# Kernel optimization log

Hardware: AMD Instinct MI355X
Metric: run time of the kernel (lower is better)

The kernel has to match this reference:

```python
import jax, jax.numpy as jnp
import numpy as np

B, DIM, NH, HD, H, W = 4, 64, 8, 8, 256, 256  # head_dim must equal num_heads (scale broadcast)


def setup_inputs() -> dict:
    key = jax.random.key(0)
    ks = jax.random.split(key, 10)
    s = 0.05
    return {
        "x": jax.random.normal(ks[0], (B, DIM, H, W), jnp.float32),
        "w3": jax.random.normal(ks[1], (DIM, 1, 3, 3), jnp.float32) * s,  # depthwise 3x3
        "b3": jax.random.normal(ks[2], (DIM,), jnp.float32) * s,
        "w5": jax.random.normal(ks[3], (DIM, 1, 5, 5), jnp.float32) * s,  # depthwise 5x5
        "b5": jax.random.normal(ks[4], (DIM,), jnp.float32) * s,
        "wqkv": jax.random.normal(ks[5], (3 * DIM, DIM), jnp.float32) * s,  # 1x1 conv, no bias
        "scale": jnp.ones((NH, 1, 1), jnp.float32),
        "g1_w": jax.random.normal(ks[6], (DIM // 4, DIM), jnp.float32) * s,
        "g1_b": jnp.zeros((DIM // 4,), jnp.float32),
        "g2_w": jax.random.normal(ks[7], (2, DIM // 4), jnp.float32) * s,
        "g2_b": jnp.zeros((2,), jnp.float32),
        "wp": jax.random.normal(ks[8], (DIM, DIM), jnp.float32) * s,  # 1x1 proj
        "bp": jnp.zeros((DIM,), jnp.float32),
    }


def _dwconv(x, w, b, pad):
    out = jax.lax.conv_general_dilated(
        x, w, (1, 1), [(pad, pad), (pad, pad)],
        dimension_numbers=("NCHW", "OIHW", "NCHW"), feature_group_count=x.shape[1])
    return out + b[None, :, None, None]


def _l2norm(t, eps=1e-12):  # F.normalize(dim=-1)
    n = jnp.sqrt(jnp.sum(t * t, axis=-1, keepdims=True))
    return t / jnp.maximum(n, eps)


def reference(x, w3, b3, w5, b5, wqkv, scale, g1_w, g1_b, g2_w, g2_b, wp, bp):
    b, c, h, w = x.shape
    conv_feat = _dwconv(x, w3, b3, 1) + _dwconv(x, w5, b5, 2)

    qkv = jnp.einsum("oc,bchw->bohw", wqkv, x)          # [b,3c,h,w]
    qkv = qkv.reshape(b, 3, NH, HD, h * w)
    q, k, v = qkv[:, 0], qkv[:, 1], qkv[:, 2]           # [b,NH,HD,hw]
    q = _l2norm(q)
    k = _l2norm(k)

    q_h = q.reshape(b, NH, HD, h, w)
    k_h = k.reshape(b, NH, HD, h, w)
    v_h = v.reshape(b, NH, HD, h, w)

    # row-axis attention: per (b,head,d-channel) attention over rows x (scale broadcasts onto HD axis)
    attn_h = jnp.einsum("bhdxy,bhdzy->bhdxz", q_h, k_h) * scale   # [b,NH,HD,h,h]
    attn_h = jax.nn.softmax(attn_h, axis=-1)
    out_h = jnp.einsum("bhdxz,bhdzy->bhdxy", attn_h, v_h).reshape(b, c, h, w)

    # column-axis attention (operate on transposed spatial layout)
    q_v = jnp.swapaxes(q_h, -1, -2)                      # [b,NH,HD,w,h]
    k_v = jnp.swapaxes(k_h, -1, -2)
    v_v = jnp.swapaxes(v_h, -1, -2)
    attn_v = jnp.einsum("bhdyx,bhdzx->bhdyz", q_v, k_v) * scale   # [b,NH,HD,w,w]
    attn_v = jax.nn.softmax(attn_v, axis=-1)
    out_v = jnp.einsum("bhdyz,bhdzx->bhdyx", attn_v, v_v)         # [b,NH,HD,w,h]
    out_v = jnp.swapaxes(out_v, -1, -2).reshape(b, c, h, w)

    attn_feat = out_h + out_v

    # global-pool gating: softmax over 2 mixing weights
    gx = jnp.mean(x, axis=(2, 3))                        # [b,c]
    h1 = jax.nn.relu(gx @ g1_w.T + g1_b)
    gw = jax.nn.softmax(h1 @ g2_w.T + g2_b, axis=1)      # [b,2]
    cw = gw[:, 0][:, None, None, None]
    aw = gw[:, 1][:, None, None, None]

    out = cw * conv_feat + aw * attn_feat
    return jnp.einsum("oc,bchw->bohw", wp, out) + bp[None, :, None, None]
```

## Files before the change

### kernel.cpp

```cpp
#include <hip/hip_runtime.h>
#include <stdint.h>


typedef unsigned short u16;
typedef __attribute__((ext_vector_type(8))) short bf16x8;
typedef __attribute__((ext_vector_type(4))) float f32x4;

#define DEV static __device__ __forceinline__

DEV u16 f2bf(float f) {
  unsigned u = __float_as_uint(f);
  return (u16)((u + 0x7fffu + ((u >> 16) & 1u)) >> 16);
}
DEV float bf2f(u16 h) { return __uint_as_float(((unsigned)h) << 16); }

DEV void bar_lds() {
  asm volatile("s_waitcnt lgkmcnt(0)" ::: "memory");
  __builtin_amdgcn_s_barrier();
}

__global__ void k_gx(const float* __restrict__ x, float* __restrict__ gxsum) {
  int bc = blockIdx.x, t = threadIdx.x;
  const float4* p = (const float4*)(x + ((size_t)bc << 16));
  float s = 0.f;
  for (int i = 0; i < 64; ++i) { float4 v = p[t + 256 * i]; s += v.x + v.y + v.z + v.w; }
  for (int off = 32; off; off >>= 1) s += __shfl_down(s, off);
  __shared__ float lds[4];
  if ((t & 63) == 0) lds[t >> 6] = s;
  __syncthreads();
  if (t == 0) gxsum[bc] = lds[0] + lds[1] + lds[2] + lds[3];
}

__global__ void k_gate(const float* __restrict__ gxsum, const float* __restrict__ g1w,
                       const float* __restrict__ g1b, const float* __restrict__ g2w,
                       const float* __restrict__ g2b, float* __restrict__ cwaw) {
  __shared__ float h1[4][16];
  int t = threadIdx.x;
  int b = t >> 4, j = t & 15;
  float a = g1b[j];
  for (int c = 0; c < 64; ++c) a += g1w[j * 64 + c] * gxsum[b * 64 + c] * (1.f / 65536.f);
  h1[b][j] = fmaxf(a, 0.f);
  __syncthreads();
  if (t < 4) {
    float l0 = g2b[0], l1 = g2b[1];
    for (int k = 0; k < 16; ++k) { l0 += g2w[k] * h1[t][k]; l1 += g2w[16 + k] * h1[t][k]; }
    float m = fmaxf(l0, l1);
    float e0 = __expf(l0 - m), e1 = __expf(l1 - m);
    float inv = 1.f / (e0 + e1);
    cwaw[t * 2 + 0] = e0 * inv;
    cwaw[t * 2 + 1] = e1 * inv;
  }
}

__global__ __launch_bounds__(256) void k_qkv(const float* __restrict__ x,
                                             const float* __restrict__ wqkv,
                                             u16* __restrict__ qkv) {
  __shared__ u16 Ws[192 * 72];
  __shared__ u16 Xs[128 * 72];
  int t = threadIdx.x;
  int b = blockIdx.x >> 9;
  int p0 = (blockIdx.x & 511) << 7;

  {
    int row = t >> 2, c0 = (t & 3) << 4;
#pragma unroll
    for (int i = 0; i < 3; ++i) {
      int r = i * 64 + row;
      const float* src = wqkv + r * 64 + c0;
      unsigned pk[8];
#pragma unroll
      for (int j = 0; j < 8; ++j)
        pk[j] = (unsigned)f2bf(src[2 * j]) | ((unsigned)f2bf(src[2 * j + 1]) << 16);
      uint4* dst = (uint4*)&Ws[r * 72 + c0];
      dst[0] = make_uint4(pk[0], pk[1], pk[2], pk[3]);
      dst[1] = make_uint4(pk[4], pk[5], pk[6], pk[7]);
    }
  }
  {
    int p = t & 127, ch = t >> 7;
    const float* xb = x + ((size_t)(b * 64) << 16) + p0 + p;
#pragma unroll
    for (int i = 0; i < 32; ++i) {
      int c = 2 * i + ch;
      Xs[p * 72 + c] = f2bf(xb[(size_t)c << 16]);
    }
  }
  __syncthreads();

  int w = t >> 6, l = t & 63, q = l >> 4, cl = l & 15;
  bf16x8 af[3][2];
#pragma unroll
  for (int g = 0; g < 3; ++g)
#pragma unroll
    for (int k = 0; k < 2; ++k)
      af[g][k] = *(const bf16x8*)&Ws[(w * 48 + g * 16 + cl) * 72 + k * 32 + q * 8];

  f32x4 acc[3][8];
  f32x4 zero = {0.f, 0.f, 0.f, 0.f};
#pragma unroll
  for (int g = 0; g < 3; ++g)
#pragma unroll
    for (int j = 0; j < 8; ++j) acc[g][j] = zero;

  for (int j = 0; j < 8; ++j) {
    bf16x8 b0 = *(const bf16x8*)&Xs[(j * 16 + cl) * 72 + q * 8];
    bf16x8 b1 = *(const bf16x8*)&Xs[(j * 16 + cl) * 72 + 32 + q * 8];
#pragma unroll
    for (int g = 0; g < 3; ++g) {
      acc[g][j] = __builtin_amdgcn_mfma_f32_16x16x32_bf16(af[g][0], b0, acc[g][j], 0, 0, 0);
      acc[g][j] = __builtin_amdgcn_mfma_f32_16x16x32_bf16(af[g][1], b1, acc[g][j], 0, 0, 0);
    }
  }
  u16* outb = qkv + ((size_t)(b * 192) << 16) + p0;
  for (int g = 0; g < 3; ++g) {
    int rowb = w * 48 + g * 16 + q * 4;
#pragma unroll
    for (int r = 0; r < 4; ++r) {
      u16* orow = outb + ((size_t)(rowb + r) << 16);
#pragma unroll
      for (int j = 0; j < 8; ++j) orow[j * 16 + cl] = f2bf(acc[g][j][r]);
    }
  }
}

__global__ void k_rnorm(const u16* __restrict__ qkv, float* __restrict__ rnorm) {
  int b = blockIdx.x >> 7, ch = blockIdx.x & 127;
  const uint2* p2 = (const uint2*)(qkv + ((size_t)(b * 192 + ch) << 16));
  int t = threadIdx.x;
  float s = 0.f;
  for (int i = 0; i < 64; ++i) {
    uint2 v = p2[t + 256 * i];
    float a = bf2f(v.x & 0xffff), bq = bf2f(v.x >> 16);
    float c = bf2f(v.y & 0xffff), d = bf2f(v.y >> 16);
    s += a * a + bq * bq + c * c + d * d;
  }
  for (int off = 32; off; off >>= 1) s += __shfl_down(s, off);
  __shared__ float lds[4];
  if ((t & 63) == 0) lds[t >> 6] = s;
  __syncthreads();
  if (t == 0) {
    float tot = lds[0] + lds[1] + lds[2] + lds[3];
    rnorm[blockIdx.x] = 1.f / fmaxf(sqrtf(tot), 1e-12f);
  }
}

__global__ void k_conv(const float* __restrict__ x, const float* __restrict__ w3,
                       const float* __restrict__ b3, const float* __restrict__ w5,
                       const float* __restrict__ b5, const float* __restrict__ cwaw,
                       float* __restrict__ outmix) {
  int rt = blockIdx.x & 31, bc = blockIdx.x >> 5, c = bc & 63, b = bc >> 6;
  int r0 = rt * 8;
  const float* xp = x + ((size_t)bc << 16);
  __shared__ float xs[12][260];
  int y = threadIdx.x;
  for (int rr = 0; rr < 12; ++rr) {
    int gr = r0 - 2 + rr;
    xs[rr][y + 2] = (gr >= 0 && gr < 256) ? xp[(size_t)gr * 256 + y] : 0.f;
  }
  if (y < 2) {
    for (int rr = 0; rr < 12; ++rr) { xs[rr][y] = 0.f; xs[rr][258 + y] = 0.f; }
  }
  __syncthreads();
  float W3[9], W5[25];
#pragma unroll
  for (int i = 0; i < 9; ++i) W3[i] = w3[c * 9 + i];
#pragma unroll
  for (int i = 0; i < 25; ++i) W5[i] = w5[c * 25 + i];
  float bias = b3[c] + b5[c];
  float cw = cwaw[b * 2];
  float* op = outmix + ((size_t)bc << 16);
  for (int k = 0; k < 8; ++k) {
    float a = bias;
#pragma unroll
    for (int di = 0; di < 3; ++di)
#pragma unroll
      for (int dj = 0; dj < 3; ++dj)
        a += W3[di * 3 + dj] * xs[k + 1 + di][y + 1 + dj];
#pragma unroll
    for (int di = 0; di < 5; ++di)
#pragma unroll
      for (int dj = 0; dj < 5; ++dj)
        a += W5[di * 5 + dj] * xs[k + di][y + dj];
    op[(size_t)(r0 + k) * 256 + y] = cw * a;
  }
}

__global__ __launch_bounds__(256) void k_attn(
    const u16* __restrict__ qkv, const float* __restrict__ rnorm,
    const float* __restrict__ scale, u16* __restrict__ oh, u16* __restrict__ ov) {
  __shared__ __align__(16) unsigned char smem[54272];
  u16* Pls = (u16*)smem;
  unsigned* Qt32 = (unsigned*)smem;
  float* red = (float*)(smem + 33792);
  unsigned* Tt32 = (unsigned*)(smem + 33792);
  float* Osf = (float*)smem;

  int t = threadIdx.x;
  int w = t >> 6, l = t & 63, q = l >> 4, cl = l & 15;
  int idx = (blockIdx.x & 7) * 256 + (blockIdx.x >> 3);
  int rt = idx & 3, dir = (idx >> 2) & 1, c = (idx >> 3) & 63, b = idx >> 9;
  int r0 = rt << 6;

  const size_t P = 65536;
  const u16* Qp = qkv + (size_t)(b * 192 + c) * P;
  const u16* Kp = qkv + (size_t)(b * 192 + 64 + c) * P;
  const u16* Vp = qkv + (size_t)(b * 192 + 128 + c) * P;

  float sc = rnorm[b * 128 + c] * rnorm[b * 128 + 64 + c] * scale[c >> 3];

  f32x4 Sa[4][4];
  f32x4 zero = {0.f, 0.f, 0.f, 0.f};
#pragma unroll
  for (int i = 0; i < 4; ++i)
#pragma unroll
    for (int j = 0; j < 4; ++j) Sa[i][j] = zero;

  if (dir == 0) {
    for (int yw = 0; yw < 8; ++yw) {
      int y0 = yw << 5;
      bf16x8 af[4], bfr[4];
#pragma unroll
      for (int i = 0; i < 4; ++i)
        af[i] = *(const bf16x8*)&Qp[(size_t)(r0 + i * 16 + cl) * 256 + y0 + q * 8];
#pragma unroll
      for (int j = 0; j < 4; ++j)
        bfr[j] = *(const bf16x8*)&Kp[(size_t)(w * 64 + j * 16 + cl) * 256 + y0 + q * 8];
      __builtin_amdgcn_s_setprio(1);
#pragma unroll
      for (int i = 0; i < 4; ++i)
#pragma unroll
        for (int j = 0; j < 4; ++j)
          Sa[i][j] = __builtin_amdgcn_mfma_f32_16x16x32_bf16(af[i], bfr[j], Sa[i][j], 0, 0, 0);
      __builtin_amdgcn_s_setprio(0);
    }
  } else {
    int y2 = t >> 4, colc = t & 15;
    int kkey = (((y2 >> 2) ^ (colc & 3)) << 2) + (y2 & 3);
    int qkey = (((y2 >> 2) ^ ((colc >> 2) & 3)) << 2) + (y2 & 3);
    unsigned KA[8], KB[8], QA[2], QB[2];
    {
      const u16* krp = Kp + (size_t)(2 * y2) * 256 + colc * 16;
      uint4 ka0 = *(const uint4*)krp;
      uint4 ka1 = *(const uint4*)(krp + 8);
      uint4 kb0 = *(const uint4*)(krp + 256);
      uint4 kb1 = *(const uint4*)(krp + 264);
      const u16* qrp = Qp + (size_t)(2 * y2) * 256 + r0 + colc * 4;
      uint2 qa = *(const uint2*)qrp;
      uint2 qb = *(const uint2*)(qrp + 256);
      KA[0] = ka0.x; KA[1] = ka0.y; KA[2] = ka0.z; KA[3] = ka0.w;
      KA[4] = ka1.x; KA[5] = ka1.y; KA[6] = ka1.z; KA[7] = ka1.w;
      KB[0] = kb0.x; KB[1] = kb0.y; KB[2] = kb0.z; KB[3] = kb0.w;
      KB[4] = kb1.x; KB[5] = kb1.y; KB[6] = kb1.z; KB[7] = kb1.w;
      QA[0] = qa.x; QA[1] = qa.y; QB[0] = qb.x; QB[1] = qb.y;
    }
#pragma unroll
    for (int yw = 0; yw < 8; ++yw) {
      bar_lds();
#pragma unroll
      for (int m = 0; m < 16; ++m) {
        unsigned lo = (m & 1) ? (KA[m >> 1] >> 16) : (KA[m >> 1] & 0xffffu);
        unsigned hi = (m & 1) ? (KB[m >> 1] & 0xffff0000u) : (KB[m >> 1] << 16);
        Tt32[(colc * 16 + m) * 20 + kkey] = lo | hi;
      }
#pragma unroll
      for (int m = 0; m < 4; ++m) {
        unsigned lo = (m & 1) ? (QA[m >> 1] >> 16) : (QA[m >> 1] & 0xffffu);
        unsigned hi = (m & 1) ? (QB[m >> 1] & 0xffff0000u) : (QB[m >> 1] << 16);
        Qt32[(colc * 4 + m) * 20 + qkey] = lo | hi;
      }
      unsigned NKA[8], NKB[8], NQA[2], NQB[2];
      if (yw < 7) {
        int y0 = (yw + 1) << 5;
        const u16* krp = Kp + (size_t)(y0 + 2 * y2) * 256 + colc * 16;
        uint4 ka0 = *(const uint4*)krp;
        uint4 ka1 = *(const uint4*)(krp + 8);
        uint4 kb0 = *(const uint4*)(krp + 256);
        uint4 kb1 = *(const uint4*)(krp + 264);
        const u16* qrp = Qp + (size_t)(y0 + 2 * y2) * 256 + r0 + colc * 4;
        uint2 qa = *(const uint2*)qrp;
        uint2 qb = *(const uint2*)(qrp + 256);
        NKA[0] = ka0.x; NKA[1] = ka0.y; NKA[2] = ka0.z; NKA[3] = ka0.w;
        NKA[4] = ka1.x; NKA[5] = ka1.y; NKA[6] = ka1.z; NKA[7] = ka1.w;
        NKB[0] = kb0.x; NKB[1] = kb0.y; NKB[2] = kb0.z; NKB[3] = kb0.w;
        NKB[4] = kb1.x; NKB[5] = kb1.y; NKB[6] = kb1.z; NKB[7] = kb1.w;
        NQA[0] = qa.x; NQA[1] = qa.y; NQB[0] = qb.x; NQB[1] = qb.y;
      }
      bar_lds();
      bf16x8 af[4], bfr[4];
#pragma unroll
      for (int i = 0; i < 4; ++i)
        af[i] = *(const bf16x8*)&Qt32[(i * 16 + cl) * 20 + ((q ^ i) << 2)];
#pragma unroll
      for (int j = 0; j < 4; ++j) {
        int col = w * 64 + j * 16 + cl;
        bfr[j] = *(const bf16x8*)&Tt32[col * 20 + ((q ^ j) << 2)];
      }
      __builtin_amdgcn_s_setprio(1);
#pragma unroll
      for (int i = 0; i < 4; ++i)
#pragma unroll
        for (int j = 0; j < 4; ++j)
          Sa[i][j] = __builtin_amdgcn_mfma_f32_16x16x32_bf16(af[i], bfr[j], Sa[i][j], 0, 0, 0);
      __builtin_amdgcn_s_setprio(0);
      if (yw < 7) {
#pragma unroll
        for (int m = 0; m < 8; ++m) { KA[m] = NKA[m]; KB[m] = NKB[m]; }
        QA[0] = NQA[0]; QA[1] = NQA[1]; QB[0] = NQB[0]; QB[1] = NQB[1];
      }
    }
    __syncthreads();
  }

  float sm[4][4];
#pragma unroll
  for (int i = 0; i < 4; ++i)
#pragma unroll
    for (int r = 0; r < 4; ++r) {
      float s0 = 0.f;
#pragma unroll
      for (int j = 0; j < 4; ++j) {
        float e = __expf(Sa[i][j][r] * sc);
        Sa[i][j][r] = e;
        s0 += e;
      }
#pragma unroll
      for (int off = 1; off < 16; off <<= 1) s0 += __shfl_xor(s0, off);
      sm[i][r] = s0;
    }
  if (cl == 0) {
#pragma unroll
    for (int i = 0; i < 4; ++i)
#pragma unroll
      for (int r = 0; r < 4; ++r) red[w * 64 + i * 16 + q * 4 + r] = sm[i][r];
  }
  __syncthreads();
#pragma unroll
  for (int i = 0; i < 4; ++i)
#pragma unroll
    for (int r = 0; r < 4; ++r) {
      int rho = i * 16 + q * 4 + r;
      sm[i][r] = 1.f / (red[rho] + red[64 + rho] + red[128 + rho] + red[192 + rho]);
    }
#pragma unroll
  for (int i = 0; i < 4; ++i)
#pragma unroll
    for (int r = 0; r < 4; ++r) {
      int rho = i * 16 + q * 4 + r;
#pragma unroll
      for (int j = 0; j < 4; ++j)
        Pls[rho * 264 + w * 64 + j * 16 + cl] = f2bf(Sa[i][j][r] * sm[i][r]);
    }
  __syncthreads();

  f32x4 Oa[4][4];
#pragma unroll
  for (int i = 0; i < 4; ++i)
#pragma unroll
    for (int j = 0; j < 4; ++j) Oa[i][j] = zero;

  if (dir == 0) {
    int z2 = t >> 4, colc = t & 15;
    int zlo = z2 & 3;
    int wkey = (((z2 >> 2) ^ (colc & 3)) << 2) + zlo;
    unsigned A[8], Bv[8];
    {
      const u16* rp = Vp + (size_t)(2 * z2) * 256 + colc * 16;
      uint4 a0 = *(const uint4*)rp;
      uint4 a1 = *(const uint4*)(rp + 8);
      uint4 c0 = *(const uint4*)(rp + 256);
      uint4 c1 = *(const uint4*)(rp + 264);
      A[0] = a0.x; A[1] = a0.y; A[2] = a0.z; A[3] = a0.w;
      A[4] = a1.x; A[5] = a1.y; A[6] = a1.z; A[7] = a1.w;
      Bv[0] = c0.x; Bv[1] = c0.y; Bv[2] = c0.z; Bv[3] = c0.w;
      Bv[4] = c1.x; Bv[5] = c1.y; Bv[6] = c1.z; Bv[7] = c1.w;
    }
#pragma unroll
    for (int zw = 0; zw < 8; ++zw) {
      int z0 = zw << 5;
      bar_lds();
#pragma unroll
      for (int m = 0; m < 16; ++m) {
        unsigned lo = (m & 1) ? (A[m >> 1] >> 16) : (A[m >> 1] & 0xffffu);
        unsigned hi = (m & 1) ? (Bv[m >> 1] & 0xffff0000u) : (Bv[m >> 1] << 16);
        Tt32[(colc * 16 + m) * 20 + wkey] = lo | hi;
      }
      unsigned NA[8], NBv[8];
      if (zw < 7) {
        const u16* rp = Vp + (size_t)(z0 + 32 + 2 * z2) * 256 + colc * 16;
        uint4 a0 = *(const uint4*)rp;
        uint4 a1 = *(const uint4*)(rp + 8);
        uint4 c0 = *(const uint4*)(rp + 256);
        uint4 c1 = *(const uint4*)(rp + 264);
        NA[0] = a0.x; NA[1] = a0.y; NA[2] = a0.z; NA[3] = a0.w;
        NA[4] = a1.x; NA[5] = a1.y; NA[6] = a1.z; NA[7] = a1.w;
        NBv[0] = c0.x; NBv[1] = c0.y; NBv[2] = c0.z; NBv[3] = c0.w;
        NBv[4] = c1.x; NBv[5] = c1.y; NBv[6] = c1.z; NBv[7] = c1.w;
      }
      bar_lds();
      bf16x8 af[4], bfr[4];
#pragma unroll
      for (int i = 0; i < 4; ++i)
        af[i] = *(const bf16x8*)&Pls[(i * 16 + cl) * 264 + z0 + q * 8];
#pragma unroll
      for (int j = 0; j < 4; ++j) {
        int col = w * 64 + j * 16 + cl;
        bfr[j] = *(const bf16x8*)&Tt32[col * 20 + ((q ^ j) << 2)];
      }
      __builtin_amdgcn_s_setprio(1);
#pragma unroll
      for (int i = 0; i < 4; ++i)
#pragma unroll
        for (int j = 0; j < 4; ++j)
          Oa[i][j] = __builtin_amdgcn_mfma_f32_16x16x32_bf16(af[i], bfr[j], Oa[i][j], 0, 0, 0);
      __builtin_amdgcn_s_setprio(0);
      if (zw < 7) {
#pragma unroll
        for (int m = 0; m < 8; ++m) { A[m] = NA[m]; Bv[m] = NBv[m]; }
      }
    }
    u16* op = oh + (size_t)(b * 64 + c) * P;
#pragma unroll
    for (int i = 0; i < 4; ++i)
#pragma unroll
      for (int j = 0; j < 4; ++j)
#pragma unroll
        for (int r = 0; r < 4; ++r)
          op[(size_t)(r0 + i * 16 + q * 4 + r) * 256 + w * 64 + j * 16 + cl] = f2bf(Oa[i][j][r]);
  } else {
    for (int zw = 0; zw < 8; ++zw) {
      int z0 = zw << 5;
      bf16x8 af[4], bfr[4];
#pragma unroll
      for (int i = 0; i < 4; ++i)
        af[i] = *(const bf16x8*)&Pls[(i * 16 + cl) * 264 + z0 + q * 8];
#pragma unroll
      for (int j = 0; j < 4; ++j)
        bfr[j] = *(const bf16x8*)&Vp[(size_t)(w * 64 + j * 16 + cl) * 256 + z0 + q * 8];
      __builtin_amdgcn_s_setprio(1);
#pragma unroll
      for (int i = 0; i < 4; ++i)
#pragma unroll
        for (int j = 0; j < 4; ++j)
          Oa[i][j] = __builtin_amdgcn_mfma_f32_16x16x32_bf16(af[i], bfr[j], Oa[i][j], 0, 0, 0);
      __builtin_amdgcn_s_setprio(0);
    }
    u16* op = ov + (size_t)(b * 64 + c) * P;
    __syncthreads();
    for (int h = 0; h < 2; ++h) {
#pragma unroll
      for (int ii = 0; ii < 2; ++ii) {
        int i = h * 2 + ii;
#pragma unroll
        for (int j = 0; j < 4; ++j)
#pragma unroll
          for (int r = 0; r < 4; ++r)
            Osf[(ii * 16 + q * 4 + r) * 260 + w * 64 + j * 16 + cl] = Oa[i][j][r];
      }
      __syncthreads();
      int rr = t & 31, xb = t >> 5;
      for (int xx = 0; xx < 32; ++xx) {
        int xcol = xx * 8 + xb;
        op[(size_t)xcol * 256 + r0 + h * 32 + rr] = f2bf(Osf[rr * 260 + xcol]);
      }
      __syncthreads();
    }
  }
}

__global__ __launch_bounds__(256) void k_final(
    float* __restrict__ dout, const u16* __restrict__ oh, const u16* __restrict__ ov,
    const float* __restrict__ wp, const float* __restrict__ bp,
    const float* __restrict__ cwaw) {
  __shared__ u16 Ms[256 * 72];
  __shared__ u16 Ws[64 * 72];
  int t = threadIdx.x;
  int b = blockIdx.x >> 8;
  int p0 = (blockIdx.x & 255) << 8;
  float aw = cwaw[b * 2 + 1];

  {
    int row = t >> 2, c0 = (t & 3) << 4;
    const float* src = wp + row * 64 + c0;
    unsigned pk[8];
#pragma unroll
    for (int j = 0; j < 8; ++j)
      pk[j] = (unsigned)f2bf(src[2 * j]) | ((unsigned)f2bf(src[2 * j + 1]) << 16);
    uint4* dst = (uint4*)&Ws[row * 72 + c0];
    dst[0] = make_uint4(pk[0], pk[1], pk[2], pk[3]);
    dst[1] = make_uint4(pk[4], pk[5], pk[6], pk[7]);
  }
  {
    size_t base = ((size_t)(b * 64) << 16) + p0 + t;
    for (int c = 0; c < 64; ++c) {
      size_t off = base + ((size_t)c << 16);
      float m = dout[off] + aw * (bf2f(oh[off]) + bf2f(ov[off]));
      Ms[t * 72 + c] = f2bf(m);
    }
  }
  __syncthreads();

  int w = t >> 6, l = t & 63, q = l >> 4, cl = l & 15;
  bf16x8 af0 = *(const bf16x8*)&Ws[(w * 16 + cl) * 72 + q * 8];
  bf16x8 af1 = *(const bf16x8*)&Ws[(w * 16 + cl) * 72 + 32 + q * 8];

  f32x4 acc[16];
  f32x4 zero = {0.f, 0.f, 0.f, 0.f};
#pragma unroll
  for (int j = 0; j < 16; ++j) acc[j] = zero;

  for (int j = 0; j < 16; ++j) {
    bf16x8 b0 = *(const bf16x8*)&Ms[(j * 16 + cl) * 72 + q * 8];
    bf16x8 b1 = *(const bf16x8*)&Ms[(j * 16 + cl) * 72 + 32 + q * 8];
    acc[j] = __builtin_amdgcn_mfma_f32_16x16x32_bf16(af0, b0, acc[j], 0, 0, 0);
    acc[j] = __builtin_amdgcn_mfma_f32_16x16x32_bf16(af1, b1, acc[j], 0, 0, 0);
  }

  float bpv[4];
#pragma unroll
  for (int r = 0; r < 4; ++r) bpv[r] = bp[w * 16 + q * 4 + r];
  float* outb = dout + ((size_t)(b * 64) << 16) + p0;
#pragma unroll
  for (int r = 0; r < 4; ++r) {
    float* orow = outb + ((size_t)(w * 16 + q * 4 + r) << 16);
#pragma unroll
    for (int j = 0; j < 16; ++j) orow[j * 16 + cl] = acc[j][r] + bpv[r];
  }
}

extern "C" void kernel_launch(void* const* d_in, const int* in_sizes, int n_in,
                              void* d_out, int out_size, void* d_ws, size_t ws_size,
                              hipStream_t stream) {
  const float* x = (const float*)d_in[0];
  const float* w3 = (const float*)d_in[1];
  const float* b3 = (const float*)d_in[2];
  const float* w5 = (const float*)d_in[3];
  const float* b5 = (const float*)d_in[4];
  const float* wqkv = (const float*)d_in[5];
  const float* scale = (const float*)d_in[6];
  const float* g1w = (const float*)d_in[7];
  const float* g1b = (const float*)d_in[8];
  const float* g2w = (const float*)d_in[9];
  const float* g2b = (const float*)d_in[10];
  const float* wp = (const float*)d_in[11];
  const float* bp = (const float*)d_in[12];
  float* out = (float*)d_out;

  char* ws = (char*)d_ws;
  u16* qkv = (u16*)(ws);
  u16* ohb = (u16*)(ws + 100663296ull);
  u16* ovb = (u16*)(ws + 134217728ull);
  float* fs = (float*)(ws + 167772160ull);
  float* gxsum = fs;
  float* cwaw = fs + 256;
  float* rnorm = fs + 264;

  k_gx<<<256, 256, 0, stream>>>(x, gxsum);
  k_gate<<<1, 64, 0, stream>>>(gxsum, g1w, g1b, g2w, g2b, cwaw);
  k_qkv<<<2048, 256, 0, stream>>>(x, wqkv, qkv);
  k_rnorm<<<512, 256, 0, stream>>>(qkv, rnorm);
  k_conv<<<8192, 256, 0, stream>>>(x, w3, b3, w5, b5, cwaw, out);
  k_attn<<<2048, 256, 0, stream>>>(qkv, rnorm, scale, ohb, ovb);
  k_final<<<1024, 256, 0, stream>>>(out, ohb, ovb, wp, bp, cwaw);
}
```

Measured before the change: 338.4 us.

## Fuse global pooling and qkv norm reductions into producer kernels via atomics

Removes the standalone global-mean kernel and q/k norm kernel. The sum of x is now accumulated inside the conv kernel from its shared tile, and squared norms are accumulated from the qkv GEMM accumulators, both with atomicAdd after a zeroing kernel. The gate weight cw is applied in the final kernel instead of conv, and that kernel's mix loads are vectorised to two pixels per thread. This avoids two extra full passes over x and over q/k, at the cost of atomic contention. The norm now comes from fp32 accumulators rather than bf16-rounded values.

```diff
diff --git a/kernel.cpp b/kernel.cpp
--- a/kernel.cpp
+++ b/kernel.cpp
@@ -19,16 +19,9 @@
   __builtin_amdgcn_s_barrier();
 }
 
-__global__ void k_gx(const float* __restrict__ x, float* __restrict__ gxsum) {
-  int bc = blockIdx.x, t = threadIdx.x;
-  const float4* p = (const float4*)(x + ((size_t)bc << 16));
-  float s = 0.f;
-  for (int i = 0; i < 64; ++i) { float4 v = p[t + 256 * i]; s += v.x + v.y + v.z + v.w; }
-  for (int off = 32; off; off >>= 1) s += __shfl_down(s, off);
-  __shared__ float lds[4];
-  if ((t & 63) == 0) lds[t >> 6] = s;
-  __syncthreads();
-  if (t == 0) gxsum[bc] = lds[0] + lds[1] + lds[2] + lds[3];
+__global__ void k_zero(float* __restrict__ fs) {
+  int t = threadIdx.x;
+  if (t < 776) fs[t] = 0.f;
 }
 
 __global__ void k_gate(const float* __restrict__ gxsum, const float* __restrict__ g1w,
@@ -54,7 +47,8 @@
 
 __global__ __launch_bounds__(256) void k_qkv(const float* __restrict__ x,
                                              const float* __restrict__ wqkv,
-                                             u16* __restrict__ qkv) {
+                                             u16* __restrict__ qkv,
+                                             float* __restrict__ rnsum) {
   __shared__ u16 Ws[192 * 72];
   __shared__ u16 Xs[128 * 72];
   int t = threadIdx.x;
@@ -121,37 +115,33 @@
       for (int j = 0; j < 8; ++j) orow[j * 16 + cl] = f2bf(acc[g][j][r]);
     }
   }
-}
-
-__global__ void k_rnorm(const u16* __restrict__ qkv, float* __restrict__ rnorm) {
-  int b = blockIdx.x >> 7, ch = blockIdx.x & 127;
-  const uint2* p2 = (const uint2*)(qkv + ((size_t)(b * 192 + ch) << 16));
-  int t = threadIdx.x;
-  float s = 0.f;
-  for (int i = 0; i < 64; ++i) {
-    uint2 v = p2[t + 256 * i];
-    float a = bf2f(v.x & 0xffff), bq = bf2f(v.x >> 16);
-    float c = bf2f(v.y & 0xffff), d = bf2f(v.y >> 16);
-    s += a * a + bq * bq + c * c + d * d;
-  }
-  for (int off = 32; off; off >>= 1) s += __shfl_down(s, off);
-  __shared__ float lds[4];
-  if ((t & 63) == 0) lds[t >> 6] = s;
-  __syncthreads();
-  if (t == 0) {
-    float tot = lds[0] + lds[1] + lds[2] + lds[3];
-    rnorm[blockIdx.x] = 1.f / fmaxf(sqrtf(tot), 1e-12f);
+  float* rn = rnsum + b * 128;
+#pragma unroll
+  for (int g = 0; g < 3; ++g) {
+    int rowb = w * 48 + g * 16 + q * 4;
+    if (rowb < 128) {
+#pragma unroll
+      for (int r = 0; r < 4; ++r) {
+        float s = 0.f;
+#pragma unroll
+        for (int j = 0; j < 8; ++j) { float v = acc[g][j][r]; s += v * v; }
+#pragma unroll
+        for (int off = 1; off < 16; off <<= 1) s += __shfl_xor(s, off);
+        if (cl == 0) atomicAdd(&rn[rowb + r], s);
+      }
+    }
   }
 }
 
 __global__ void k_conv(const float* __restrict__ x, const float* __restrict__ w3,
                        const float* __restrict__ b3, const float* __restrict__ w5,
-                       const float* __restrict__ b5, const float* __restrict__ cwaw,
-                       float* __restrict__ outmix) {
-  int rt = blockIdx.x & 31, bc = blockIdx.x >> 5, c = bc & 63, b = bc >> 6;
+                       const float* __restrict__ b5, float* __restrict__ outmix,
+                       float* __restrict__ gxsum) {
+  int rt = blockIdx.x & 31, bc = blockIdx.x >> 5, c = bc & 63;
   int r0 = rt * 8;
   const float* xp = x + ((size_t)bc << 16);
   __shared__ float xs[12][260];
+  __shared__ float redg[4];
   int y = threadIdx.x;
   for (int rr = 0; rr < 12; ++rr) {
     int gr = r0 - 2 + rr;
@@ -167,7 +157,6 @@
 #pragma unroll
   for (int i = 0; i < 25; ++i) W5[i] = w5[c * 25 + i];
   float bias = b3[c] + b5[c];
-  float cw = cwaw[b * 2];
   float* op = outmix + ((size_t)bc << 16);
   for (int k = 0; k < 8; ++k) {
     float a = bias;
@@ -181,12 +170,19 @@
 #pragma unroll
       for (int dj = 0; dj < 5; ++dj)
         a += W5[di * 5 + dj] * xs[k + di][y + dj];
-    op[(size_t)(r0 + k) * 256 + y] = cw * a;
-  }
+    op[(size_t)(r0 + k) * 256 + y] = a;
+  }
+  float s = 0.f;
+#pragma unroll
+  for (int k = 0; k < 8; ++k) s += xs[k + 2][y + 2];
+  for (int off = 32; off; off >>= 1) s += __shfl_down(s, off);
+  if ((y & 63) == 0) redg[y >> 6] = s;
+  __syncthreads();
+  if (y == 0) atomicAdd(&gxsum[bc], redg[0] + redg[1] + redg[2] + redg[3]);
 }
 
 __global__ __launch_bounds__(256) void k_attn(
-    const u16* __restrict__ qkv, const float* __restrict__ rnorm,
+    const u16* __restrict__ qkv, const float* __restrict__ rnsum,
     const float* __restrict__ scale, u16* __restrict__ oh, u16* __restrict__ ov) {
   __shared__ __align__(16) unsigned char smem[54272];
   u16* Pls = (u16*)smem;
@@ -206,7 +202,8 @@
   const u16* Kp = qkv + (size_t)(b * 192 + 64 + c) * P;
   const u16* Vp = qkv + (size_t)(b * 192 + 128 + c) * P;
 
-  float sc = rnorm[b * 128 + c] * rnorm[b * 128 + 64 + c] * scale[c >> 3];
+  float sq = rnsum[b * 128 + c], sk = rnsum[b * 128 + 64 + c];
+  float sc = scale[c >> 3] / (fmaxf(sqrtf(sq), 1e-12f) * fmaxf(sqrtf(sk), 1e-12f));
 
   f32x4 Sa[4][4];
   f32x4 zero = {0.f, 0.f, 0.f, 0.f};
@@ -476,7 +473,7 @@
   int t = threadIdx.x;
   int b = blockIdx.x >> 8;
   int p0 = (blockIdx.x & 255) << 8;
-  float aw = cwaw[b * 2 + 1];
+  float cw = cwaw[b * 2], aw = cwaw[b * 2 + 1];
 
   {
     int row = t >> 2, c0 = (t & 3) << 4;
@@ -490,11 +487,18 @@
     dst[1] = make_uint4(pk[4], pk[5], pk[6], pk[7]);
   }
   {
-    size_t base = ((size_t)(b * 64) << 16) + p0 + t;
-    for (int c = 0; c < 64; ++c) {
-      size_t off = base + ((size_t)c << 16);
-      float m = dout[off] + aw * (bf2f(oh[off]) + bf2f(ov[off]));
-      Ms[t * 72 + c] = f2bf(m);
+    int p2 = (t & 127) * 2, ch0 = (t >> 7) * 32;
+    size_t base = ((size_t)(b * 64 + ch0) << 16) + p0 + p2;
+    for (int cc = 0; cc < 32; ++cc) {
+      size_t off = base + ((size_t)cc << 16);
+      float2 dv = *(const float2*)&dout[off];
+      unsigned ohv = *(const unsigned*)&oh[off];
+      unsigned ovv = *(const unsigned*)&ov[off];
+      int c = ch0 + cc;
+      float m0 = cw * dv.x + aw * (bf2f((u16)(ohv & 0xffff)) + bf2f((u16)(ovv & 0xffff)));
+      float m1 = cw * dv.y + aw * (bf2f((u16)(ohv >> 16)) + bf2f((u16)(ovv >> 16)));
+      Ms[p2 * 72 + c] = f2bf(m0);
+      Ms[(p2 + 1) * 72 + c] = f2bf(m1);
     }
   }
   __syncthreads();
@@ -552,13 +556,12 @@
   float* fs = (float*)(ws + 167772160ull);
   float* gxsum = fs;
   float* cwaw = fs + 256;
-  float* rnorm = fs + 264;
-
-  k_gx<<<256, 256, 0, stream>>>(x, gxsum);
+  float* rnsum = fs + 264;
+
+  k_zero<<<1, 1024, 0, stream>>>(fs);
+  k_qkv<<<2048, 256, 0, stream>>>(x, wqkv, qkv, rnsum);
+  k_conv<<<8192, 256, 0, stream>>>(x, w3, b3, w5, b5, out, gxsum);
   k_gate<<<1, 64, 0, stream>>>(gxsum, g1w, g1b, g2w, g2b, cwaw);
-  k_qkv<<<2048, 256, 0, stream>>>(x, wqkv, qkv);
-  k_rnorm<<<512, 256, 0, stream>>>(qkv, rnorm);
-  k_conv<<<8192, 256, 0, stream>>>(x, w3, b3, w5, b5, cwaw, out);
-  k_attn<<<2048, 256, 0, stream>>>(qkv, rnorm, scale, ohb, ovb);
+  k_attn<<<2048, 256, 0, stream>>>(qkv, rnsum, scale, ohb, ovb);
   k_final<<<1024, 256, 0, stream>>>(out, ohb, ovb, wp, bp, cwaw);
 }
```

After: 533.8 us. 57.7% more time.

## Fuse q/k norm reduction into QKV GEMM epilogue via striped atomics

Applied to the files above, without the earlier changes.

Removes the separate k_rnorm pass, which re-read all q and k channels from global memory. The QKV GEMM epilogue now computes per-channel sums of squares from fp32 accumulators and atomically adds them into 16 stripes of partial sums, which k_attn sums and turns into the norm scale. The partial sums live in the output buffer, cleared by a new k_zero kernel, so k_attn must run before k_conv overwrites it; the launch order is changed to match. Norms now come from unrounded fp32 values rather than the stored bf16, and atomic float adds make the result order-dependent.

```diff
diff --git a/kernel.cpp b/kernel.cpp
--- a/kernel.cpp
+++ b/kernel.cpp
@@ -17,6 +17,11 @@
 DEV void bar_lds() {
   asm volatile("s_waitcnt lgkmcnt(0)" ::: "memory");
   __builtin_amdgcn_s_barrier();
+}
+
+__global__ void k_zero(float* __restrict__ rns) {
+  int i = blockIdx.x * 1024 + threadIdx.x;
+  if (i < 8192) rns[i] = 0.f;
 }
 
 __global__ void k_gx(const float* __restrict__ x, float* __restrict__ gxsum) {
@@ -54,7 +59,8 @@
 
 __global__ __launch_bounds__(256) void k_qkv(const float* __restrict__ x,
                                              const float* __restrict__ wqkv,
-                                             u16* __restrict__ qkv) {
+                                             u16* __restrict__ qkv,
+                                             float* __restrict__ rns) {
   __shared__ u16 Ws[192 * 72];
   __shared__ u16 Xs[128 * 72];
   int t = threadIdx.x;
@@ -121,26 +127,21 @@
       for (int j = 0; j < 8; ++j) orow[j * 16 + cl] = f2bf(acc[g][j][r]);
     }
   }
-}
-
-__global__ void k_rnorm(const u16* __restrict__ qkv, float* __restrict__ rnorm) {
-  int b = blockIdx.x >> 7, ch = blockIdx.x & 127;
-  const uint2* p2 = (const uint2*)(qkv + ((size_t)(b * 192 + ch) << 16));
-  int t = threadIdx.x;
-  float s = 0.f;
-  for (int i = 0; i < 64; ++i) {
-    uint2 v = p2[t + 256 * i];
-    float a = bf2f(v.x & 0xffff), bq = bf2f(v.x >> 16);
-    float c = bf2f(v.y & 0xffff), d = bf2f(v.y >> 16);
-    s += a * a + bq * bq + c * c + d * d;
-  }
-  for (int off = 32; off; off >>= 1) s += __shfl_down(s, off);
-  __shared__ float lds[4];
-  if ((t & 63) == 0) lds[t >> 6] = s;
-  __syncthreads();
-  if (t == 0) {
-    float tot = lds[0] + lds[1] + lds[2] + lds[3];
-    rnorm[blockIdx.x] = 1.f / fmaxf(sqrtf(tot), 1e-12f);
+  float* rn = rns + (blockIdx.x & 15) * 512 + b * 128;
+#pragma unroll
+  for (int g = 0; g < 3; ++g) {
+    int rowb = w * 48 + g * 16 + q * 4;
+    if (rowb < 128) {
+#pragma unroll
+      for (int r = 0; r < 4; ++r) {
+        float s = 0.f;
+#pragma unroll
+        for (int j = 0; j < 8; ++j) { float v = acc[g][j][r]; s += v * v; }
+#pragma unroll
+        for (int off = 1; off < 16; off <<= 1) s += __shfl_xor(s, off);
+        if (cl == 0) atomicAdd(&rn[rowb + r], s);
+      }
+    }
   }
 }
 
@@ -186,7 +187,7 @@
 }
 
 __global__ __launch_bounds__(256) void k_attn(
-    const u16* __restrict__ qkv, const float* __restrict__ rnorm,
+    const u16* __restrict__ qkv, const float* __restrict__ rns,
     const float* __restrict__ scale, u16* __restrict__ oh, u16* __restrict__ ov) {
   __shared__ __align__(16) unsigned char smem[54272];
   u16* Pls = (u16*)smem;
@@ -206,7 +207,13 @@
   const u16* Kp = qkv + (size_t)(b * 192 + 64 + c) * P;
   const u16* Vp = qkv + (size_t)(b * 192 + 128 + c) * P;
 
-  float sc = rnorm[b * 128 + c] * rnorm[b * 128 + 64 + c] * scale[c >> 3];
+  float sq = 0.f, sk = 0.f;
+#pragma unroll
+  for (int s = 0; s < 16; ++s) {
+    sq += rns[s * 512 + b * 128 + c];
+    sk += rns[s * 512 + b * 128 + 64 + c];
+  }
+  float sc = scale[c >> 3] / (fmaxf(sqrtf(sq), 1e-12f) * fmaxf(sqrtf(sk), 1e-12f));
 
   f32x4 Sa[4][4];
   f32x4 zero = {0.f, 0.f, 0.f, 0.f};
@@ -552,13 +559,13 @@
   float* fs = (float*)(ws + 167772160ull);
   float* gxsum = fs;
   float* cwaw = fs + 256;
-  float* rnorm = fs + 264;
-
+  float* rns = (float*)d_out;
+
+  k_zero<<<8, 1024, 0, stream>>>(rns);
+  k_qkv<<<2048, 256, 0, stream>>>(x, wqkv, qkv, rns);
   k_gx<<<256, 256, 0, stream>>>(x, gxsum);
   k_gate<<<1, 64, 0, stream>>>(gxsum, g1w, g1b, g2w, g2b, cwaw);
-  k_qkv<<<2048, 256, 0, stream>>>(x, wqkv, qkv);
-  k_rnorm<<<512, 256, 0, stream>>>(qkv, rnorm);
+  k_attn<<<2048, 256, 0, stream>>>(qkv, rns, scale, ohb, ovb);
   k_conv<<<8192, 256, 0, stream>>>(x, w3, b3, w5, b5, cwaw, out);
-  k_attn<<<2048, 256, 0, stream>>>(qkv, rnorm, scale, ohb, ovb);
   k_final<<<1024, 256, 0, stream>>>(out, ohb, ovb, wp, bp, cwaw);
 }
```

After: 377.6 us. 1.12x slower.
